# Kernel optimization log

Hardware: AMD Instinct MI355X
Metric: run time of the kernel (lower is better)

The kernel has to match this reference:

```python
import jax, jax.numpy as jnp
import numpy as np

N_TOKENS = 4096
HIDDEN = 2048
INTER = 1024
N_EXPERTS = 8          # routed experts
ZERO_EXPERTS = 2       # Longcat zero-computation (identity) experts
TOP_K = 2
ROUTED_SCALING = 2.5


def setup_inputs() -> dict:
    key = jax.random.key(0)
    k1, k2, k3, k4 = jax.random.split(key, 4)
    hidden_states = jax.random.normal(k1, (N_TOKENS, HIDDEN), dtype=jnp.float32)
    router_w = jax.random.normal(k2, (N_EXPERTS + ZERO_EXPERTS, HIDDEN), dtype=jnp.float32) * 0.02
    correction_bias = jnp.zeros((N_EXPERTS + ZERO_EXPERTS,), dtype=jnp.float32)
    # torch Linear weight layout [out, in]: gate_up [E, 2I, H], down [E, H, I]
    w_gate_up = jax.random.normal(k3, (N_EXPERTS, 2 * INTER, HIDDEN), dtype=jnp.float32) * 0.02
    w_down = jax.random.normal(k4, (N_EXPERTS, HIDDEN, INTER), dtype=jnp.float32) * 0.02
    return {
        'hidden_states': hidden_states,
        'router_w': router_w,
        'correction_bias': correction_bias,
        'w_gate_up': w_gate_up,
        'w_down': w_down,
    }


def reference(hidden_states, router_w, correction_bias, w_gate_up, w_down):
    x = hidden_states  # [N, H]
    # ---- router gemm (fp32, like dsv3_router_gemm) ----
    logits = jnp.einsum('nh,eh->ne', x.astype(jnp.float32), router_w)  # [N, E+Z]
    scores = jax.nn.sigmoid(logits)
    # biased top-k selection (sglang biased topk, renormalize=False)
    _, topk_idx = jax.lax.top_k(scores + correction_bias[None, :], TOP_K)  # [N, K]
    topk_w = jnp.take_along_axis(scores, topk_idx, axis=1)  # raw sigmoid scores
    # ---- combine weights per expert ----
    onehot = jax.nn.one_hot(topk_idx, N_EXPERTS + ZERO_EXPERTS, dtype=topk_w.dtype)  # [N,K,E+Z]
    combine = jnp.einsum('nke,nk->ne', onehot, topk_w)  # [N, E+Z]
    combine_real = combine[:, :N_EXPERTS]               # [N, E]
    w_zero = combine[:, N_EXPERTS:].sum(axis=-1)        # [N] identity-expert weight
    # ---- expert FFN (silu(gate) * up -> down), dense over experts ----
    gu = jnp.einsum('nh,efh->enf', x, w_gate_up)        # [E, N, 2I]
    gate, up = gu[..., :INTER], gu[..., INTER:]
    h = jax.nn.silu(gate) * up                          # [E, N, I]
    y = jnp.einsum('eni,ehi->enh', h, w_down)           # [E, N, H]
    out = jnp.einsum('enh,ne->nh', y, combine_real.astype(y.dtype))
    out = out + w_zero[:, None].astype(out.dtype) * x   # zero experts = identity
    return out * ROUTED_SCALING
```

## Files before the change

kernel.cpp:

```cpp
#include <hip/hip_runtime.h>
#include <cstdint>
#include <cstddef>

#define N_TOKENS 4096
#define HIDDEN   2048
#define INTER    1024
#define NE       8
#define NE_TOT   10
#define SCALE    2.5f

typedef short v8s __attribute__((ext_vector_type(8)));
typedef float v4f __attribute__((ext_vector_type(4)));

static __device__ inline int imin(int a, int b) { return a < b ? a : b; }

__device__ inline unsigned short f2bf(float f) {
  unsigned int u = __float_as_uint(f);
  u += 0x7fffu + ((u >> 16) & 1u);
  return (unsigned short)(u >> 16);
}

__device__ inline void gld_lds16(const void* g, void* l) {
  __builtin_amdgcn_global_load_lds(
      (const __attribute__((address_space(1))) unsigned int*)g,
      (__attribute__((address_space(3))) unsigned int*)l, 16, 0, 0);
}

__global__ __launch_bounds__(256) void cvt_all_kernel(
    const float* __restrict__ wgu, const float* __restrict__ wd,
    unsigned short* __restrict__ wgu_b, unsigned short* __restrict__ wd_b) {
  int i = blockIdx.x * 256 + threadIdx.x;
  const int n8_gu = NE * 2 * INTER * HIDDEN / 8;
  const int n8_d  = NE * HIDDEN * INTER / 8;
  const float* src;
  unsigned short* dst;
  size_t b;
  if (i < n8_gu)            { src = wgu; dst = wgu_b; b = (size_t)i * 8; }
  else if (i < n8_gu + n8_d){ src = wd;  dst = wd_b;  b = (size_t)(i - n8_gu) * 8; }
  else return;
  float4 a0 = *(const float4*)(src + b);
  float4 a1 = *(const float4*)(src + b + 4);
  union { unsigned short u[8]; uint4 v; } r;
  r.u[0] = f2bf(a0.x); r.u[1] = f2bf(a0.y); r.u[2] = f2bf(a0.z); r.u[3] = f2bf(a0.w);
  r.u[4] = f2bf(a1.x); r.u[5] = f2bf(a1.y); r.u[6] = f2bf(a1.z); r.u[7] = f2bf(a1.w);
  *(uint4*)(dst + b) = r.v;
}

__global__ __launch_bounds__(256, 4) void router_kernel(
    const float* __restrict__ x, const float* __restrict__ rw,
    const float* __restrict__ bias, unsigned short* __restrict__ xb,
    signed char* __restrict__ tke, float* __restrict__ tkw,
    float* __restrict__ out) {
  int tid  = threadIdx.x;
  int lane = tid & 63;
  int wid  = tid >> 6;
  int n    = blockIdx.x * 4 + wid;

  const float* xr = x + (size_t)n * HIDDEN;
  float acc[NE_TOT];
#pragma unroll
  for (int e = 0; e < NE_TOT; e++) acc[e] = 0.f;

#pragma unroll 1
  for (int i = 0; i < 8; i++) {
    int k = (i * 64 + lane) * 4;
    float4 xv = *(const float4*)(xr + k);
#pragma unroll
    for (int e = 0; e < NE_TOT; e++) {
      float4 w = *(const float4*)(rw + (size_t)e * HIDDEN + k);
      acc[e] += xv.x * w.x + xv.y * w.y + xv.z * w.z + xv.w * w.w;
    }
  }
#pragma unroll
  for (int e = 0; e < NE_TOT; e++) {
    float v = acc[e];
#pragma unroll
    for (int off = 32; off > 0; off >>= 1) v += __shfl_xor(v, off, 64);
    acc[e] = v;
  }

  float sc[NE_TOT], sb[NE_TOT];
#pragma unroll
  for (int e = 0; e < NE_TOT; e++) {
    sc[e] = 1.f / (1.f + expf(-acc[e]));
    sb[e] = sc[e] + bias[e];
  }
  int i1 = 0;
  for (int e = 1; e < NE_TOT; e++) if (sb[e] > sb[i1]) i1 = e;
  int i2 = (i1 == 0) ? 1 : 0;
  for (int e = 0; e < NE_TOT; e++) if (e != i1 && sb[e] > sb[i2]) i2 = e;
  float wzero = 0.f;
  if (i1 >= NE) wzero += sc[i1];
  if (i2 >= NE) wzero += sc[i2];
  if (lane == 0) {
    tke[n]            = (signed char)(i1 < NE ? i1 : -1);
    tke[N_TOKENS + n] = (signed char)(i2 < NE ? i2 : -1);
    tkw[n]            = i1 < NE ? SCALE * sc[i1] : 0.f;
    tkw[N_TOKENS + n] = i2 < NE ? SCALE * sc[i2] : 0.f;
  }
  float wz = SCALE * wzero;

#pragma unroll
  for (int i = 0; i < 8; i++) {
    int k = (i * 64 + lane) * 4;
    float4 xv = *(const float4*)(xr + k);
    ushort4 ob;
    ob.x = f2bf(xv.x); ob.y = f2bf(xv.y);
    ob.z = f2bf(xv.z); ob.w = f2bf(xv.w);
    *(ushort4*)(xb + (size_t)n * HIDDEN + k) = ob;
    float4 o;
    o.x = wz * xv.x; o.y = wz * xv.y; o.z = wz * xv.z; o.w = wz * xv.w;
    *(float4*)(out + (size_t)n * HIDDEN + k) = o;
  }
}

__global__ __launch_bounds__(1024) void partition_kernel(
    const signed char* __restrict__ tke, int* __restrict__ tok_list,
    int* __restrict__ tkr, int* __restrict__ counts, int* __restrict__ offsets) {
  __shared__ int scn[1024][NE];
  __shared__ int soff[NE];
  int tid = threadIdx.x;
  int t4  = tid * 4;

  int w0 = *(const int*)(tke + t4);
  int w1 = *(const int*)(tke + N_TOKENS + t4);

#pragma unroll
  for (int e = 0; e < NE; e++) scn[tid][e] = 0;
#pragma unroll
  for (int i = 0; i < 4; i++) {
    int e0 = (int)(signed char)(w0 >> (8 * i));
    int e1 = (int)(signed char)(w1 >> (8 * i));
    if (e0 >= 0) scn[tid][e0]++;
    if (e1 >= 0) scn[tid][e1]++;
  }
  int c[NE], orig[NE];
#pragma unroll
  for (int e = 0; e < NE; e++) { c[e] = scn[tid][e]; orig[e] = c[e]; }
  __syncthreads();

  for (int s = 1; s < 1024; s <<= 1) {
    int v[NE];
    bool act = (tid >= s);
    if (act) {
#pragma unroll
      for (int e = 0; e < NE; e++) v[e] = scn[tid - s][e];
    }
    __syncthreads();
    if (act) {
#pragma unroll
      for (int e = 0; e < NE; e++) { c[e] += v[e]; scn[tid][e] = c[e]; }
    }
    __syncthreads();
  }

  if (tid == 0) {
    int s = 0;
#pragma unroll
    for (int e = 0; e < NE; e++) {
      int cnt = scn[1023][e];
      counts[e] = cnt; offsets[e] = s; soff[e] = s; s += cnt;
    }
  }
  __syncthreads();

#pragma unroll
  for (int e = 0; e < NE; e++) scn[tid][e] = c[e] - orig[e];

#pragma unroll
  for (int i = 0; i < 4; i++) {
    int n  = t4 + i;
    int e0 = (int)(signed char)(w0 >> (8 * i));
    int e1 = (int)(signed char)(w1 >> (8 * i));
    if (e0 >= 0) {
      int slot = scn[tid][e0]++;
      tok_list[e0 * N_TOKENS + slot] = n;
      tkr[n] = soff[e0] + slot;
    } else tkr[n] = 0;
    if (e1 >= 0) {
      int slot = scn[tid][e1]++;
      tok_list[e1 * N_TOKENS + slot] = n;
      tkr[N_TOKENS + n] = soff[e1] + slot;
    } else tkr[N_TOKENS + n] = 0;
  }
}


__global__ __launch_bounds__(256, 2) void gateup_kernel(
    const unsigned short* __restrict__ xb, const unsigned short* __restrict__ wgu,
    const int* __restrict__ counts, const int* __restrict__ offsets,
    const int* __restrict__ tok_list, unsigned short* __restrict__ h_buf) {
  int jt = blockIdx.x;
  int mt = blockIdx.y;
  int e  = blockIdx.z;
  int count = counts[e];
  if (mt * 128 >= count) return;

  __shared__ unsigned short As[2][128 * 32];
  __shared__ unsigned short Bs[2][128 * 32];

  int tid  = threadIdx.x;
  int lane = tid & 63;
  int wm = (tid >> 7) & 1;
  int wn = (tid >> 6) & 1;

  int row0 = tid >> 2, row1 = row0 + 64;
  int col8 = (((tid & 3) ^ ((tid >> 3) & 3)) * 8);

  const int* tl = tok_list + e * N_TOKENS;
  int t0 = tl[imin(mt * 128 + row0, count - 1)];
  int t1 = tl[imin(mt * 128 + row1, count - 1)];
  const unsigned short* ag0 = xb + (size_t)t0 * HIDDEN + col8;
  const unsigned short* ag1 = xb + (size_t)t1 * HIDDEN + col8;

  int wn0 = row0 >> 6, wi0 = row0 & 63;
  int wn1 = row1 >> 6, wi1 = row1 & 63;
  int br0 = (wi0 < 32) ? (jt * 64 + wn0 * 32 + wi0) : (1024 + jt * 64 + wn0 * 32 + (wi0 - 32));
  int br1 = (wi1 < 32) ? (jt * 64 + wn1 * 32 + wi1) : (1024 + jt * 64 + wn1 * 32 + (wi1 - 32));
  const unsigned short* bbase = wgu + (size_t)e * (2 * INTER) * HIDDEN;
  const unsigned short* bg0 = bbase + (size_t)br0 * HIDDEN + col8;
  const unsigned short* bg1 = bbase + (size_t)br1 * HIDDEN + col8;

  v4f acc[4][4];
#pragma unroll
  for (int i = 0; i < 4; i++)
#pragma unroll
    for (int j = 0; j < 4; j++) acc[i][j] = v4f{0.f, 0.f, 0.f, 0.f};

  int mrow = wm * 64 + (lane & 15);
  int nrow = wn * 64 + (lane & 15);
  int kcol = (((lane >> 4) ^ ((lane >> 1) & 3)) * 8);

  gld_lds16(ag0, &As[0][(size_t)tid * 8]);
  gld_lds16(ag1, &As[0][2048 + (size_t)tid * 8]);
  gld_lds16(bg0, &Bs[0][(size_t)tid * 8]);
  gld_lds16(bg1, &Bs[0][2048 + (size_t)tid * 8]);
  ag0 += 32; ag1 += 32; bg0 += 32; bg1 += 32;
  __syncthreads();

  const int NK = HIDDEN / 32;
  for (int kt = 0; kt < NK; kt++) {
    int cur = kt & 1;
    if (kt + 1 < NK) {
      int nxt = cur ^ 1;
      gld_lds16(ag0, &As[nxt][(size_t)tid * 8]);
      gld_lds16(ag1, &As[nxt][2048 + (size_t)tid * 8]);
      gld_lds16(bg0, &Bs[nxt][(size_t)tid * 8]);
      gld_lds16(bg1, &Bs[nxt][2048 + (size_t)tid * 8]);
      ag0 += 32; ag1 += 32; bg0 += 32; bg1 += 32;
    }
    v8s a[4], b[4];
#pragma unroll
    for (int i = 0; i < 4; i++) a[i] = *(const v8s*)&As[cur][(mrow + i * 16) * 32 + kcol];
#pragma unroll
    for (int j = 0; j < 4; j++) b[j] = *(const v8s*)&Bs[cur][(nrow + j * 16) * 32 + kcol];
#pragma unroll
    for (int i = 0; i < 4; i++)
#pragma unroll
      for (int j = 0; j < 4; j++)
        acc[i][j] = __builtin_amdgcn_mfma_f32_16x16x32_bf16(a[i], b[j], acc[i][j], 0, 0, 0);
    __syncthreads();
  }

  int ocol  = lane & 15;
  int orow4 = (lane >> 4) * 4;
  int hoff  = offsets[e];
#pragma unroll
  for (int i = 0; i < 4; i++) {
#pragma unroll
    for (int r = 0; r < 4; r++) {
      int m = mt * 128 + wm * 64 + i * 16 + orow4 + r;
      if (m < count) {
        unsigned short* hrow = h_buf + (size_t)(hoff + m) * INTER;
#pragma unroll
        for (int j = 0; j < 2; j++) {
          float g = acc[i][j][r];
          float u = acc[i][j + 2][r];
          float hv = (g / (1.f + expf(-g))) * u;
          hrow[jt * 64 + wn * 32 + j * 16 + ocol] = f2bf(hv);
        }
      }
    }
  }
}

__global__ __launch_bounds__(256, 2) void down_kernel(
    const unsigned short* __restrict__ h_buf, const unsigned short* __restrict__ wd,
    const int* __restrict__ counts, const int* __restrict__ offsets,
    float* __restrict__ y_buf) {
  int nt = blockIdx.x;
  int mt = blockIdx.y;
  int e  = blockIdx.z;
  int count = counts[e];
  if (mt * 128 >= count) return;

  __shared__ unsigned short As[2][128 * 32];
  __shared__ unsigned short Bs[2][128 * 32];

  int tid  = threadIdx.x;
  int lane = tid & 63;
  int wm = (tid >> 7) & 1;
  int wn = (tid >> 6) & 1;

  int row0 = tid >> 2, row1 = row0 + 64;
  int col8 = (((tid & 3) ^ ((tid >> 3) & 3)) * 8);
  int hoff = offsets[e];

  const unsigned short* ag0 =
      h_buf + (size_t)(hoff + imin(mt * 128 + row0, count - 1)) * INTER + col8;
  const unsigned short* ag1 =
      h_buf + (size_t)(hoff + imin(mt * 128 + row1, count - 1)) * INTER + col8;
  const unsigned short* bbase = wd + (size_t)e * HIDDEN * INTER;
  const unsigned short* bg0 = bbase + (size_t)(nt * 128 + row0) * INTER + col8;
  const unsigned short* bg1 = bbase + (size_t)(nt * 128 + row1) * INTER + col8;

  v4f acc[4][4];
#pragma unroll
  for (int i = 0; i < 4; i++)
#pragma unroll
    for (int j = 0; j < 4; j++) acc[i][j] = v4f{0.f, 0.f, 0.f, 0.f};

  int mrow = wm * 64 + (lane & 15);
  int nrow = wn * 64 + (lane & 15);
  int kcol = (((lane >> 4) ^ ((lane >> 1) & 3)) * 8);

  gld_lds16(ag0, &As[0][(size_t)tid * 8]);
  gld_lds16(ag1, &As[0][2048 + (size_t)tid * 8]);
  gld_lds16(bg0, &Bs[0][(size_t)tid * 8]);
  gld_lds16(bg1, &Bs[0][2048 + (size_t)tid * 8]);
  ag0 += 32; ag1 += 32; bg0 += 32; bg1 += 32;
  __syncthreads();

  const int NK = INTER / 32;
  for (int kt = 0; kt < NK; kt++) {
    int cur = kt & 1;
    if (kt + 1 < NK) {
      int nxt = cur ^ 1;
      gld_lds16(ag0, &As[nxt][(size_t)tid * 8]);
      gld_lds16(ag1, &As[nxt][2048 + (size_t)tid * 8]);
      gld_lds16(bg0, &Bs[nxt][(size_t)tid * 8]);
      gld_lds16(bg1, &Bs[nxt][2048 + (size_t)tid * 8]);
      ag0 += 32; ag1 += 32; bg0 += 32; bg1 += 32;
    }
    v8s a[4], b[4];
#pragma unroll
    for (int i = 0; i < 4; i++) a[i] = *(const v8s*)&As[cur][(mrow + i * 16) * 32 + kcol];
#pragma unroll
    for (int j = 0; j < 4; j++) b[j] = *(const v8s*)&Bs[cur][(nrow + j * 16) * 32 + kcol];
#pragma unroll
    for (int i = 0; i < 4; i++)
#pragma unroll
      for (int j = 0; j < 4; j++)
        acc[i][j] = __builtin_amdgcn_mfma_f32_16x16x32_bf16(a[i], b[j], acc[i][j], 0, 0, 0);
    __syncthreads();
  }

  int ocol  = lane & 15;
  int orow4 = (lane >> 4) * 4;
#pragma unroll
  for (int i = 0; i < 4; i++) {
#pragma unroll
    for (int r = 0; r < 4; r++) {
      int m = mt * 128 + wm * 64 + i * 16 + orow4 + r;
      if (m < count) {
        float* yrow = y_buf + (size_t)(hoff + m) * HIDDEN + nt * 128 + wn * 64 + ocol;
#pragma unroll
        for (int j = 0; j < 4; j++) yrow[j * 16] = acc[i][j][r];
      }
    }
  }
}

__global__ __launch_bounds__(256, 4) void gather_kernel(
    const float* __restrict__ y_buf, const int* __restrict__ tkr,
    const float* __restrict__ tkw, float* __restrict__ out) {
  int tid  = threadIdx.x;
  int lane = tid & 63;
  int wid  = tid >> 6;
  int n    = blockIdx.x * 4 + wid;

  int r1 = tkr[n], r2 = tkr[N_TOKENS + n];
  float w1 = tkw[n], w2 = tkw[N_TOKENS + n];
  const float* y1 = y_buf + (size_t)r1 * HIDDEN;
  const float* y2 = y_buf + (size_t)r2 * HIDDEN;
  float* orow = out + (size_t)n * HIDDEN;

#pragma unroll
  for (int i = 0; i < 8; i++) {
    int k = (i * 64 + lane) * 4;
    float4 o = *(const float4*)(orow + k);
    float4 a = *(const float4*)(y1 + k);
    float4 b = *(const float4*)(y2 + k);
    o.x += w1 * a.x + w2 * b.x;
    o.y += w1 * a.y + w2 * b.y;
    o.z += w1 * a.z + w2 * b.z;
    o.w += w1 * a.w + w2 * b.w;
    *(float4*)(orow + k) = o;
  }
}

extern "C" void kernel_launch(void* const* d_in, const int* in_sizes, int n_in,
                              void* d_out, int out_size, void* d_ws, size_t ws_size,
                              hipStream_t stream) {
  const float* x   = (const float*)d_in[0];
  const float* rw  = (const float*)d_in[1];
  const float* cb  = (const float*)d_in[2];
  const float* wgu = (const float*)d_in[3];
  const float* wd  = (const float*)d_in[4];
  float* out = (float*)d_out;

  char* ws = (char*)d_ws;
  size_t off = 0;
  auto alloc = [&](size_t bytes) {
    void* p = ws + off;
    off += (bytes + 255) & ~(size_t)255;
    return p;
  };
  unsigned short* xb    = (unsigned short*)alloc((size_t)N_TOKENS * HIDDEN * 2);
  unsigned short* wgu_b = (unsigned short*)alloc((size_t)NE * 2 * INTER * HIDDEN * 2);
  unsigned short* wd_b  = (unsigned short*)alloc((size_t)NE * HIDDEN * INTER * 2);
  unsigned short* h_buf = (unsigned short*)alloc((size_t)2 * N_TOKENS * INTER * 2);
  int*   tok_list = (int*)alloc((size_t)NE * N_TOKENS * 4);
  signed char* tke = (signed char*)alloc((size_t)2 * N_TOKENS);
  int*   tkr      = (int*)alloc((size_t)2 * N_TOKENS * 4);
  float* tkw      = (float*)alloc((size_t)2 * N_TOKENS * 4);
  int*   counts   = (int*)alloc(256);
  int*   offsets  = (int*)alloc(256);
  float* y_buf = (float*)wgu_b;
  (void)ws_size; (void)in_sizes; (void)n_in; (void)out_size;

  const int n8_total = (NE * 2 * INTER * HIDDEN + NE * HIDDEN * INTER) / 8;
  cvt_all_kernel<<<(n8_total + 255) / 256, 256, 0, stream>>>(wgu, wd, wgu_b, wd_b);
  router_kernel<<<N_TOKENS / 4, 256, 0, stream>>>(x, rw, cb, xb, tke, tkw, out);
  partition_kernel<<<1, 1024, 0, stream>>>(tke, tok_list, tkr, counts, offsets);
  gateup_kernel<<<dim3(16, 32, 8), 256, 0, stream>>>(xb, wgu_b, counts, offsets, tok_list, h_buf);
  down_kernel<<<dim3(16, 32, 8), 256, 0, stream>>>(h_buf, wd_b, counts, offsets, y_buf);
  gather_kernel<<<N_TOKENS / 4, 256, 0, stream>>>(y_buf, tkr, tkw, out);
}
```

Measured before the change: 459.8 us.

## Fuse fp32-to-bf16 weight conversion into expert GEMM tile loads

Removes the separate weight conversion kernel and instead loads fp32 weights directly in the gate-up and down GEMMs, converting to bf16 in registers before writing to shared memory. This avoids a full read/write pass over all expert weights. In exchange, weight tiles are re-read in fp32 (twice the bytes) by every token tile, and the B loads go through registers synchronously rather than async global-to-LDS. Launch bounds are raised to allow more resident blocks.

```diff
diff --git a/kernel.cpp b/kernel.cpp
--- a/kernel.cpp
+++ b/kernel.cpp
@@ -20,30 +20,17 @@
   return (unsigned short)(u >> 16);
 }
 
+__device__ inline uint4 f2bf8(float4 a0, float4 a1) {
+  union { unsigned short u[8]; uint4 v; } r;
+  r.u[0] = f2bf(a0.x); r.u[1] = f2bf(a0.y); r.u[2] = f2bf(a0.z); r.u[3] = f2bf(a0.w);
+  r.u[4] = f2bf(a1.x); r.u[5] = f2bf(a1.y); r.u[6] = f2bf(a1.z); r.u[7] = f2bf(a1.w);
+  return r.v;
+}
+
 __device__ inline void gld_lds16(const void* g, void* l) {
   __builtin_amdgcn_global_load_lds(
       (const __attribute__((address_space(1))) unsigned int*)g,
       (__attribute__((address_space(3))) unsigned int*)l, 16, 0, 0);
-}
-
-__global__ __launch_bounds__(256) void cvt_all_kernel(
-    const float* __restrict__ wgu, const float* __restrict__ wd,
-    unsigned short* __restrict__ wgu_b, unsigned short* __restrict__ wd_b) {
-  int i = blockIdx.x * 256 + threadIdx.x;
-  const int n8_gu = NE * 2 * INTER * HIDDEN / 8;
-  const int n8_d  = NE * HIDDEN * INTER / 8;
-  const float* src;
-  unsigned short* dst;
-  size_t b;
-  if (i < n8_gu)            { src = wgu; dst = wgu_b; b = (size_t)i * 8; }
-  else if (i < n8_gu + n8_d){ src = wd;  dst = wd_b;  b = (size_t)(i - n8_gu) * 8; }
-  else return;
-  float4 a0 = *(const float4*)(src + b);
-  float4 a1 = *(const float4*)(src + b + 4);
-  union { unsigned short u[8]; uint4 v; } r;
-  r.u[0] = f2bf(a0.x); r.u[1] = f2bf(a0.y); r.u[2] = f2bf(a0.z); r.u[3] = f2bf(a0.w);
-  r.u[4] = f2bf(a1.x); r.u[5] = f2bf(a1.y); r.u[6] = f2bf(a1.z); r.u[7] = f2bf(a1.w);
-  *(uint4*)(dst + b) = r.v;
 }
 
 __global__ __launch_bounds__(256, 4) void router_kernel(
@@ -186,8 +173,8 @@
 }
 
 
-__global__ __launch_bounds__(256, 2) void gateup_kernel(
-    const unsigned short* __restrict__ xb, const unsigned short* __restrict__ wgu,
+__global__ __launch_bounds__(256, 4) void gateup_kernel(
+    const unsigned short* __restrict__ xb, const float* __restrict__ wgu,
     const int* __restrict__ counts, const int* __restrict__ offsets,
     const int* __restrict__ tok_list, unsigned short* __restrict__ h_buf) {
   int jt = blockIdx.x;
@@ -217,9 +204,9 @@
   int wn1 = row1 >> 6, wi1 = row1 & 63;
   int br0 = (wi0 < 32) ? (jt * 64 + wn0 * 32 + wi0) : (1024 + jt * 64 + wn0 * 32 + (wi0 - 32));
   int br1 = (wi1 < 32) ? (jt * 64 + wn1 * 32 + wi1) : (1024 + jt * 64 + wn1 * 32 + (wi1 - 32));
-  const unsigned short* bbase = wgu + (size_t)e * (2 * INTER) * HIDDEN;
-  const unsigned short* bg0 = bbase + (size_t)br0 * HIDDEN + col8;
-  const unsigned short* bg1 = bbase + (size_t)br1 * HIDDEN + col8;
+  const float* bbase = wgu + (size_t)e * (2 * INTER) * HIDDEN;
+  const float* bg0 = bbase + (size_t)br0 * HIDDEN + col8;
+  const float* bg1 = bbase + (size_t)br1 * HIDDEN + col8;
 
   v4f acc[4][4];
 #pragma unroll
@@ -231,11 +218,20 @@
   int nrow = wn * 64 + (lane & 15);
   int kcol = (((lane >> 4) ^ ((lane >> 1) & 3)) * 8);
 
-  gld_lds16(ag0, &As[0][(size_t)tid * 8]);
-  gld_lds16(ag1, &As[0][2048 + (size_t)tid * 8]);
-  gld_lds16(bg0, &Bs[0][(size_t)tid * 8]);
-  gld_lds16(bg1, &Bs[0][2048 + (size_t)tid * 8]);
-  ag0 += 32; ag1 += 32; bg0 += 32; bg1 += 32;
+#define GU_STAGE(buf)                                                        \
+  do {                                                                       \
+    gld_lds16(ag0, &As[buf][(size_t)tid * 8]);                               \
+    gld_lds16(ag1, &As[buf][2048 + (size_t)tid * 8]);                        \
+    float4 c0 = *(const float4*)bg0;                                         \
+    float4 c1 = *(const float4*)(bg0 + 4);                                   \
+    float4 d0 = *(const float4*)bg1;                                         \
+    float4 d1 = *(const float4*)(bg1 + 4);                                   \
+    *(uint4*)&Bs[buf][(size_t)tid * 8] = f2bf8(c0, c1);                      \
+    *(uint4*)&Bs[buf][2048 + (size_t)tid * 8] = f2bf8(d0, d1);               \
+    ag0 += 32; ag1 += 32; bg0 += 32; bg1 += 32;                              \
+  } while (0)
+
+  GU_STAGE(0);
   __syncthreads();
 
   const int NK = HIDDEN / 32;
@@ -243,11 +239,7 @@
     int cur = kt & 1;
     if (kt + 1 < NK) {
       int nxt = cur ^ 1;
-      gld_lds16(ag0, &As[nxt][(size_t)tid * 8]);
-      gld_lds16(ag1, &As[nxt][2048 + (size_t)tid * 8]);
-      gld_lds16(bg0, &Bs[nxt][(size_t)tid * 8]);
-      gld_lds16(bg1, &Bs[nxt][2048 + (size_t)tid * 8]);
-      ag0 += 32; ag1 += 32; bg0 += 32; bg1 += 32;
+      GU_STAGE(nxt);
     }
     v8s a[4], b[4];
 #pragma unroll
@@ -261,6 +253,7 @@
         acc[i][j] = __builtin_amdgcn_mfma_f32_16x16x32_bf16(a[i], b[j], acc[i][j], 0, 0, 0);
     __syncthreads();
   }
+#undef GU_STAGE
 
   int ocol  = lane & 15;
   int orow4 = (lane >> 4) * 4;
@@ -284,8 +277,8 @@
   }
 }
 
-__global__ __launch_bounds__(256, 2) void down_kernel(
-    const unsigned short* __restrict__ h_buf, const unsigned short* __restrict__ wd,
+__global__ __launch_bounds__(256, 4) void down_kernel(
+    const unsigned short* __restrict__ h_buf, const float* __restrict__ wd,
     const int* __restrict__ counts, const int* __restrict__ offsets,
     float* __restrict__ y_buf) {
   int nt = blockIdx.x;
@@ -310,9 +303,9 @@
       h_buf + (size_t)(hoff + imin(mt * 128 + row0, count - 1)) * INTER + col8;
   const unsigned short* ag1 =
       h_buf + (size_t)(hoff + imin(mt * 128 + row1, count - 1)) * INTER + col8;
-  const unsigned short* bbase = wd + (size_t)e * HIDDEN * INTER;
-  const unsigned short* bg0 = bbase + (size_t)(nt * 128 + row0) * INTER + col8;
-  const unsigned short* bg1 = bbase + (size_t)(nt * 128 + row1) * INTER + col8;
+  const float* bbase = wd + (size_t)e * HIDDEN * INTER;
+  const float* bg0 = bbase + (size_t)(nt * 128 + row0) * INTER + col8;
+  const float* bg1 = bbase + (size_t)(nt * 128 + row1) * INTER + col8;
 
   v4f acc[4][4];
 #pragma unroll
@@ -324,11 +317,20 @@
   int nrow = wn * 64 + (lane & 15);
   int kcol = (((lane >> 4) ^ ((lane >> 1) & 3)) * 8);
 
-  gld_lds16(ag0, &As[0][(size_t)tid * 8]);
-  gld_lds16(ag1, &As[0][2048 + (size_t)tid * 8]);
-  gld_lds16(bg0, &Bs[0][(size_t)tid * 8]);
-  gld_lds16(bg1, &Bs[0][2048 + (size_t)tid * 8]);
-  ag0 += 32; ag1 += 32; bg0 += 32; bg1 += 32;
+#define DN_STAGE(buf)                                                        \
+  do {                                                                       \
+    gld_lds16(ag0, &As[buf][(size_t)tid * 8]);                               \
+    gld_lds16(ag1, &As[buf][2048 + (size_t)tid * 8]);                        \
+    float4 c0 = *(const float4*)bg0;                                         \
+    float4 c1 = *(const float4*)(bg0 + 4);                                   \
+    float4 d0 = *(const float4*)bg1;                                         \
+    float4 d1 = *(const float4*)(bg1 + 4);                                   \
+    *(uint4*)&Bs[buf][(size_t)tid * 8] = f2bf8(c0, c1);                      \
+    *(uint4*)&Bs[buf][2048 + (size_t)tid * 8] = f2bf8(d0, d1);               \
+    ag0 += 32; ag1 += 32; bg0 += 32; bg1 += 32;                              \
+  } while (0)
+
+  DN_STAGE(0);
   __syncthreads();
 
   const int NK = INTER / 32;
@@ -336,11 +338,7 @@
     int cur = kt & 1;
     if (kt + 1 < NK) {
       int nxt = cur ^ 1;
-      gld_lds16(ag0, &As[nxt][(size_t)tid * 8]);
-      gld_lds16(ag1, &As[nxt][2048 + (size_t)tid * 8]);
-      gld_lds16(bg0, &Bs[nxt][(size_t)tid * 8]);
-      gld_lds16(bg1, &Bs[nxt][2048 + (size_t)tid * 8]);
-      ag0 += 32; ag1 += 32; bg0 += 32; bg1 += 32;
+      DN_STAGE(nxt);
     }
     v8s a[4], b[4];
 #pragma unroll
@@ -354,6 +352,7 @@
         acc[i][j] = __builtin_amdgcn_mfma_f32_16x16x32_bf16(a[i], b[j], acc[i][j], 0, 0, 0);
     __syncthreads();
   }
+#undef DN_STAGE
 
   int ocol  = lane & 15;
   int orow4 = (lane >> 4) * 4;
@@ -417,23 +416,19 @@
     return p;
   };
   unsigned short* xb    = (unsigned short*)alloc((size_t)N_TOKENS * HIDDEN * 2);
-  unsigned short* wgu_b = (unsigned short*)alloc((size_t)NE * 2 * INTER * HIDDEN * 2);
-  unsigned short* wd_b  = (unsigned short*)alloc((size_t)NE * HIDDEN * INTER * 2);
   unsigned short* h_buf = (unsigned short*)alloc((size_t)2 * N_TOKENS * INTER * 2);
+  float* y_buf          = (float*)alloc((size_t)2 * N_TOKENS * HIDDEN * 4);
   int*   tok_list = (int*)alloc((size_t)NE * N_TOKENS * 4);
   signed char* tke = (signed char*)alloc((size_t)2 * N_TOKENS);
   int*   tkr      = (int*)alloc((size_t)2 * N_TOKENS * 4);
   float* tkw      = (float*)alloc((size_t)2 * N_TOKENS * 4);
   int*   counts   = (int*)alloc(256);
   int*   offsets  = (int*)alloc(256);
-  float* y_buf = (float*)wgu_b;
   (void)ws_size; (void)in_sizes; (void)n_in; (void)out_size;
 
-  const int n8_total = (NE * 2 * INTER * HIDDEN + NE * HIDDEN * INTER) / 8;
-  cvt_all_kernel<<<(n8_total + 255) / 256, 256, 0, stream>>>(wgu, wd, wgu_b, wd_b);
   router_kernel<<<N_TOKENS / 4, 256, 0, stream>>>(x, rw, cb, xb, tke, tkw, out);
   partition_kernel<<<1, 1024, 0, stream>>>(tke, tok_list, tkr, counts, offsets);
-  gateup_kernel<<<dim3(16, 32, 8), 256, 0, stream>>>(xb, wgu_b, counts, offsets, tok_list, h_buf);
-  down_kernel<<<dim3(16, 32, 8), 256, 0, stream>>>(h_buf, wd_b, counts, offsets, y_buf);
+  gateup_kernel<<<dim3(16, 32, 8), 256, 0, stream>>>(xb, wgu, counts, offsets, tok_list, h_buf);
+  down_kernel<<<dim3(16, 32, 8), 256, 0, stream>>>(h_buf, wd, counts, offsets, y_buf);
   gather_kernel<<<N_TOKENS / 4, 256, 0, stream>>>(y_buf, tkr, tkw, out);
 }
```

Result: no change. 468.3 us (+1.8%).
